# Kernel tuning notes

Measured on AMD Instinct MI355X. Metric: run time of the kernel, lower is better.

The kernel has to match this reference:

```python
import jax, jax.numpy as jnp
import numpy as np

_GELU = lambda x: jax.nn.gelu(x, approximate=False)  # torch nn.GELU default = exact erf


def setup_inputs():
    key = jax.random.key(0)
    ks = jax.random.split(key, 32)
    B, H = 16384, 768
    def p(i, shape):
        return jax.random.normal(ks[i], shape, jnp.float32) * 0.02
    return {
        "image_feat": jax.random.normal(ks[0], (B, H), jnp.float32),
        "text_feat": jax.random.normal(ks[1], (B, H), jnp.float32),
        "enhanced_image_feat": jax.random.normal(ks[2], (B, H), jnp.float32),
        "enhanced_text_feat": jax.random.normal(ks[3], (B, H), jnp.float32),
        "missing_type": jax.random.randint(ks[4], (B,), 0, 4),
        # info_encoder: H->256->64
        "info_w1": p(5, (H, 256)), "info_b1": jnp.zeros((256,), jnp.float32),
        "info_w2": p(6, (256, 64)), "info_b2": jnp.zeros((64,), jnp.float32),
        # modality_importance_predictor: H->H/2->1 (dropout inactive at eval)
        "imp_w1": p(7, (H, H // 2)), "imp_b1": jnp.zeros((H // 2,), jnp.float32),
        "imp_w2": p(8, (H // 2, 1)), "imp_b2": jnp.zeros((1,), jnp.float32),
        # feature_discriminator: H->256->64->1
        "disc_w1": p(9, (H, 256)), "disc_b1": jnp.zeros((256,), jnp.float32),
        "disc_w2": p(10, (256, 64)), "disc_b2": jnp.zeros((64,), jnp.float32),
        "disc_w3": p(11, (64, 1)), "disc_b3": jnp.zeros((1,), jnp.float32),
        # consistency_predictor: 2H->H->H/2->1
        "cons_w1": p(12, (2 * H, H)), "cons_b1": jnp.zeros((H,), jnp.float32),
        "cons_w2": p(13, (H, H // 2)), "cons_b2": jnp.zeros((H // 2,), jnp.float32),
        "cons_w3": p(14, (H // 2, 1)), "cons_b3": jnp.zeros((1,), jnp.float32),
        # task_difficulty_predictor: 2H->H->H/2->1
        "diff_w1": p(15, (2 * H, H)), "diff_b1": jnp.zeros((H,), jnp.float32),
        "diff_w2": p(16, (H, H // 2)), "diff_b2": jnp.zeros((H // 2,), jnp.float32),
        "diff_w3": p(17, (H // 2, 1)), "diff_b3": jnp.zeros((1,), jnp.float32),
    }


def _forward(image_feat, text_feat, enhanced_image_feat, enhanced_text_feat,
             info_w1, info_b1, info_w2, info_b2,
             imp_w1, imp_b1, imp_w2, imp_b2,
             disc_w1, disc_b1, disc_w2, disc_b2, disc_w3, disc_b3,
             cons_w1, cons_b1, cons_w2, cons_b2, cons_w3, cons_b3,
             diff_w1, diff_b1, diff_w2, diff_b2, diff_w3, diff_b3):
    sig = jax.nn.sigmoid

    def geometric(f):  # vectorized version of the per-sample python loop
        n = jnp.linalg.norm(f, axis=-1)
        nq = sig((n - 1.0) * 2.0)
        sp = jnp.mean((jnp.abs(f) > 0.01).astype(jnp.float32), axis=-1)
        sq = sig(jnp.std(f, axis=-1, ddof=1) * 10.0 - 1.0)  # torch.std is unbiased
        return (nq + sp + sq) / 3.0

    def information(f):
        enc = _GELU(f @ info_w1 + info_b1) @ info_w2 + info_b2  # [B,64]
        disc = jnp.round(sig(enc) * 10.0).astype(jnp.int32)     # values in 0..10
        # histogram-based entropy == the torch.unique loop (prob = count/64)
        counts = jnp.sum(disc[:, :, None] == jnp.arange(11, dtype=jnp.int32)[None, None, :], axis=1)
        prob = counts.astype(jnp.float32) / enc.shape[-1]
        ent = -jnp.sum(jnp.where(prob > 0, prob * jnp.log(prob + 1e-8), 0.0), axis=-1)
        eq = sig(ent - 2.0)
        # svd of a 1xD matrix has a single singular value = ||f||_2
        n = jnp.linalg.norm(f, axis=-1)
        cq = (n > 0.01).astype(jnp.float32) / f.shape[-1]
        fn = f / jnp.maximum(n, 1e-12)[:, None]  # F.normalize
        dq = sig(jnp.sum(fn * fn, axis=-1) - 0.5)
        return (eq + cq + dq) / 3.0

    def importance(f):
        return sig(_GELU(f @ imp_w1 + imp_b1) @ imp_w2 + imp_b2)[:, 0]

    def discrim(f):
        h = _GELU(f @ disc_w1 + disc_b1)
        h = _GELU(h @ disc_w2 + disc_b2)
        return sig(h @ disc_w3 + disc_b3)[:, 0]

    def head3(f, w1, b1, w2, b2, w3, b3):
        h = _GELU(f @ w1 + b1)
        h = _GELU(h @ w2 + b2)
        return sig(h @ w3 + b3)[:, 0]

    g_img = geometric(image_feat)
    g_txt = geometric(text_feat)
    g_eimg = geometric(enhanced_image_feat)
    g_etxt = geometric(enhanced_text_feat)
    i_img = information(image_feat)
    i_txt = information(text_feat)
    cons_o = head3(jnp.concatenate([image_feat, text_feat], -1), cons_w1, cons_b1, cons_w2, cons_b2, cons_w3, cons_b3)
    cons_e = head3(jnp.concatenate([enhanced_image_feat, enhanced_text_feat], -1), cons_w1, cons_b1, cons_w2, cons_b2, cons_w3, cons_b3)
    imp_i = importance(image_feat)
    imp_t = importance(text_feat)
    imp_ei = importance(enhanced_image_feat)
    imp_et = importance(enhanced_text_feat)
    auth_io = discrim(image_feat)
    auth_ie = discrim(enhanced_image_feat)
    auth_to = discrim(text_feat)
    auth_te = discrim(enhanced_text_feat)
    diff = head3(jnp.concatenate([enhanced_image_feat, enhanced_text_feat], -1), diff_w1, diff_b1, diff_w2, diff_b2, diff_w3, diff_b3)
    overall = (g_img + g_txt + i_img + i_txt + cons_e + (imp_i + imp_t) / 2.0) / 6.0
    return jnp.stack([g_img, g_txt, g_eimg, g_etxt, i_img, i_txt, cons_o, cons_e,
                      imp_i, imp_t, imp_ei, imp_et, auth_io, auth_ie, auth_to, auth_te,
                      diff, overall])  # [18, B]


def reference(image_feat, text_feat, enhanced_image_feat, enhanced_text_feat, missing_type,
              info_w1, info_b1, info_w2, info_b2,
              imp_w1, imp_b1, imp_w2, imp_b2,
              disc_w1, disc_b1, disc_w2, disc_b2, disc_w3, disc_b3,
              cons_w1, cons_b1, cons_w2, cons_b2, cons_w3, cons_b3,
              diff_w1, diff_b1, diff_w2, diff_b2, diff_w3, diff_b3):
    # missing_type is carried by the original forward but never used in the math
    return _forward(image_feat, text_feat, enhanced_image_feat, enhanced_text_feat,
                    info_w1, info_b1, info_w2, info_b2,
                    imp_w1, imp_b1, imp_w2, imp_b2,
                    disc_w1, disc_b1, disc_w2, disc_b2, disc_w3, disc_b3,
                    cons_w1, cons_b1, cons_w2, cons_b2, cons_w3, cons_b3,
                    diff_w1, diff_b1, diff_w2, diff_b2, diff_w3, diff_b3)
```

## Files before the change

kernel.cpp:

```cpp
#include <hip/hip_runtime.h>

typedef unsigned short bfu;
typedef __attribute__((ext_vector_type(8))) __bf16 bf16x8;
typedef __attribute__((ext_vector_type(4))) float f32x4;

__device__ __forceinline__ float bf2f(bfu u) {
    unsigned int x = ((unsigned int)u) << 16;
    return __builtin_bit_cast(float, x);
}
__device__ __forceinline__ bfu f2bf(float f) {
    unsigned int u = __builtin_bit_cast(unsigned int, f);
    unsigned int r = (u + 0x7fffu + ((u >> 16) & 1u)) >> 16;
    return (bfu)r;
}
__device__ __forceinline__ float sigm(float x) { return 1.0f / (1.0f + __expf(-x)); }
__device__ __forceinline__ float gelu_f(float x) {
    const float y = 0.7978845608f * (x + 0.044715f * x * x * x);
    const float t = 1.f - 2.f / (__expf(2.f * y) + 1.f);
    return 0.5f * x * (1.f + t);
}
__device__ __forceinline__ float gelu_x(float x) {
    return 0.5f * x * (1.0f + erff(x * 0.70710678118654752f));
}

__device__ __forceinline__ void async16(const void* g, void* l) {
    __builtin_amdgcn_global_load_lds((const __attribute__((address_space(1))) void*)g,
                                     (__attribute__((address_space(3))) void*)l, 16, 0, 0);
}

struct TDesc { const float* src; bfu* dst; int K, N, blk0; };
struct TPack { TDesc d[9]; };

__global__ __launch_bounds__(256) void transpose_k(TPack p) {
    const int bid = blockIdx.x;
    int j = 0;
#pragma unroll
    for (int i = 1; i < 9; ++i)
        if (bid >= p.d[i].blk0) j = i;
    const TDesc d = p.d[j];
    const int local = bid - d.blk0;
    const int tkn = d.K >> 6;
    const int tk = local % tkn, tn = local / tkn;
    const int k0 = tk * 64, n0 = tn * 64;
    __shared__ float tile[64][65];
    const int tx = threadIdx.x & 63, ty = threadIdx.x >> 6;
#pragma unroll
    for (int i = 0; i < 16; ++i) {
        const int r = ty * 16 + i;
        tile[r][tx] = d.src[(size_t)(k0 + r) * d.N + n0 + tx];
    }
    __syncthreads();
#pragma unroll
    for (int i = 0; i < 16; ++i) {
        const int n = ty * 16 + i;
        d.dst[(size_t)(n0 + n) * d.K + k0 + tx] = f2bf(tile[tx][n]);
    }
}

__global__ __launch_bounds__(256)
void geomcast_k(const float* F0, const float* F1, bfu* D0, bfu* D1,
                float* g0, float* g1, float* p0, float* p1) {
    const int z = blockIdx.y;
    const float* F = z ? F1 : F0;
    bfu* D = z ? D1 : D0;
    float* gout = z ? g1 : g0;
    float* part = z ? p1 : p0;
    const int wave = threadIdx.x >> 6, lane = threadIdx.x & 63;
    const int row = blockIdx.x * 4 + wave;
    const float* fr = F + (size_t)row * 768;
    bfu* dr = D + (size_t)row * 768;
    float sum = 0.f, ss = 0.f, cnt = 0.f;
#pragma unroll
    for (int i = 0; i < 3; ++i) {
        const float4 v = *(const float4*)(fr + i * 256 + lane * 4);
        sum += v.x + v.y + v.z + v.w;
        ss += v.x * v.x + v.y * v.y + v.z * v.z + v.w * v.w;
        cnt += ((fabsf(v.x) > 0.01f) ? 1.f : 0.f) + ((fabsf(v.y) > 0.01f) ? 1.f : 0.f) +
               ((fabsf(v.z) > 0.01f) ? 1.f : 0.f) + ((fabsf(v.w) > 0.01f) ? 1.f : 0.f);
        ushort4 b;
        b.x = f2bf(v.x); b.y = f2bf(v.y); b.z = f2bf(v.z); b.w = f2bf(v.w);
        *(ushort4*)(dr + i * 256 + lane * 4) = b;
    }
#pragma unroll
    for (int off = 32; off; off >>= 1) {
        sum += __shfl_xor(sum, off);
        ss  += __shfl_xor(ss, off);
        cnt += __shfl_xor(cnt, off);
    }
    if (lane == 0) {
        const float n = sqrtf(ss);
        const float nq = sigm((n - 1.f) * 2.f);
        const float sp = cnt * (1.f / 768.f);
        float var = (ss - sum * sum * (1.f / 768.f)) * (1.f / 767.f);
        var = fmaxf(var, 0.f);
        const float sq = sigm(sqrtf(var) * 10.f - 1.f);
        gout[row] = (nq + sp + sq) * (1.f / 3.f);
        if (part) {
            const float cq = (n > 0.01f) ? (1.f / 768.f) : 0.f;
            const float nc = fmaxf(n, 1e-12f);
            const float dq = sigm(ss / (nc * nc) - 0.5f);
            part[row] = (cq + dq) * (1.f / 3.f);
        }
    }
}

struct Seg {
    const bfu* A; const bfu* A2;
    const bfu* W;
    const float* bias;
    const float* dotw;
    bfu* C;
    float* acc;
    int ldc; int mode;
};
struct SegPack { Seg s[12]; };

__global__ __launch_bounds__(256)
void gemm_k(SegPack p, int K, int Ksplit, int lda) {
    constexpr int BM = 128, BK = 64, MT = 4, NT = 4;
    __shared__ bfu As[BM * BK];
    __shared__ bfu Ws[128 * BK];
    const int NTt = gridDim.x;
    const int g = blockIdx.y * NTt + blockIdx.x;
    const int G8 = NTt * 8;
    const int m = (g / G8) * 8 + (g & 7);
    const int n = (g % G8) >> 3;
    const Seg sg = p.s[n];
    const int t = threadIdx.x;
    const int wave = t >> 6, lane = t & 63;
    const int row_l = lane & 15, kq = lane >> 4;
    const int m0 = m * BM;
    const int wm = wave >> 1, wn = wave & 1;
    const int wrow0 = wm * 64, wcol0 = wn * 64;

    f32x4 acc[MT][NT] = {};

    const int nkt = K / BK;
    for (int kt = 0; kt < nkt; ++kt) {
        const int k0 = kt * BK;
        const bfu* Ab;
        int kc;
        if (k0 < Ksplit) { Ab = sg.A; kc = k0; }
        else             { Ab = sg.A2; kc = k0 - Ksplit; }
#pragma unroll
        for (int i = 0; i < 4; ++i) {
            const int c = i * 256 + t;
            const int r = c >> 3, s = c & 7;
            const int cc = (s ^ (r & 7)) << 3;
            async16(Ab + (size_t)(m0 + r) * lda + kc + cc, As + ((i * 256 + wave * 64) << 3));
        }
#pragma unroll
        for (int i = 0; i < 4; ++i) {
            const int c = i * 256 + t;
            const int r = c >> 3, s = c & 7;
            const int cc = (s ^ (r & 7)) << 3;
            async16(sg.W + (size_t)r * K + k0 + cc, Ws + ((i * 256 + wave * 64) << 3));
        }
        __syncthreads();
#pragma unroll
        for (int ks = 0; ks < 2; ++ks) {
            bf16x8 af[MT], bfr[NT];
#pragma unroll
            for (int mi = 0; mi < MT; ++mi) {
                const int rA = wrow0 + mi * 16 + row_l;
                af[mi] = *(const bf16x8*)(As + rA * BK + (((ks * 4 + kq) ^ (rA & 7)) << 3));
            }
#pragma unroll
            for (int ni = 0; ni < NT; ++ni) {
                const int rB = wcol0 + ni * 16 + row_l;
                bfr[ni] = *(const bf16x8*)(Ws + rB * BK + (((ks * 4 + kq) ^ (rB & 7)) << 3));
            }
#pragma unroll
            for (int mi = 0; mi < MT; ++mi)
#pragma unroll
                for (int ni = 0; ni < NT; ++ni)
                    acc[mi][ni] = __builtin_amdgcn_mfma_f32_16x16x32_bf16(af[mi], bfr[ni], acc[mi][ni], 0, 0, 0);
        }
        __syncthreads();
    }

    if (sg.mode == 0) {
#pragma unroll
        for (int ni = 0; ni < NT; ++ni) {
            const int col = wcol0 + ni * 16 + row_l;
            const float bv = sg.bias[col];
#pragma unroll
            for (int mi = 0; mi < MT; ++mi)
#pragma unroll
                for (int r = 0; r < 4; ++r) {
                    const int row = m0 + wrow0 + mi * 16 + kq * 4 + r;
                    sg.C[(size_t)row * sg.ldc + col] = f2bf(gelu_f(acc[mi][ni][r] + bv));
                }
        }
    } else if (sg.mode == 2) {
#pragma unroll
        for (int ni = 0; ni < NT; ++ni) {
            const int col = wcol0 + ni * 16 + row_l;
            const float bv = sg.bias[col];
#pragma unroll
            for (int mi = 0; mi < MT; ++mi)
#pragma unroll
                for (int r = 0; r < 4; ++r) {
                    const int row = m0 + wrow0 + mi * 16 + kq * 4 + r;
                    sg.C[(size_t)row * sg.ldc + col] = f2bf(gelu_x(acc[mi][ni][r] + bv));
                }
        }
    } else {
#pragma unroll
        for (int mi = 0; mi < MT; ++mi)
#pragma unroll
            for (int r = 0; r < 4; ++r) {
                float s = 0.f;
#pragma unroll
                for (int ni = 0; ni < NT; ++ni) {
                    const int col = wcol0 + ni * 16 + row_l;
                    s += sg.dotw[col] * gelu_f(acc[mi][ni][r] + sg.bias[col]);
                }
                s += __shfl_xor(s, 1); s += __shfl_xor(s, 2);
                s += __shfl_xor(s, 4); s += __shfl_xor(s, 8);
                if (row_l == 0)
                    atomicAdd(sg.acc + m0 + wrow0 + mi * 16 + kq * 4 + r, s);
            }
    }
}

__global__ __launch_bounds__(256)
void gemm64dot_k(const bfu* __restrict__ A, const bfu* __restrict__ W,
                 const float* __restrict__ bias, const float* __restrict__ dotw,
                 float* acc_out, int K, int lda) {
    constexpr int BK = 64, MT = 2, NT = 4;
    __shared__ bfu As[128 * BK];
    __shared__ bfu Ws[64 * BK];
    const int t = threadIdx.x;
    const int wave = t >> 6, lane = t & 63;
    const int row_l = lane & 15, kq = lane >> 4;
    const int m0 = blockIdx.x * 128;
    const int wrow0 = wave * 32;
    f32x4 acc[MT][NT] = {};
    const int nkt = K / BK;
    for (int kt = 0; kt < nkt; ++kt) {
        const int k0 = kt * BK;
#pragma unroll
        for (int i = 0; i < 4; ++i) {
            const int c = i * 256 + t;
            const int r = c >> 3, s = c & 7;
            const int cc = (s ^ (r & 7)) << 3;
            async16(A + (size_t)(m0 + r) * lda + k0 + cc, As + ((i * 256 + wave * 64) << 3));
        }
#pragma unroll
        for (int i = 0; i < 2; ++i) {
            const int c = i * 256 + t;
            const int r = c >> 3, s = c & 7;
            const int cc = (s ^ (r & 7)) << 3;
            async16(W + (size_t)r * K + k0 + cc, Ws + ((i * 256 + wave * 64) << 3));
        }
        __syncthreads();
#pragma unroll
        for (int ks = 0; ks < 2; ++ks) {
            bf16x8 af[MT], bfr[NT];
#pragma unroll
            for (int mi = 0; mi < MT; ++mi) {
                const int rA = wrow0 + mi * 16 + row_l;
                af[mi] = *(const bf16x8*)(As + rA * BK + (((ks * 4 + kq) ^ (rA & 7)) << 3));
            }
#pragma unroll
            for (int ni = 0; ni < NT; ++ni) {
                const int rB = ni * 16 + row_l;
                bfr[ni] = *(const bf16x8*)(Ws + rB * BK + (((ks * 4 + kq) ^ (rB & 7)) << 3));
            }
#pragma unroll
            for (int mi = 0; mi < MT; ++mi)
#pragma unroll
                for (int ni = 0; ni < NT; ++ni)
                    acc[mi][ni] = __builtin_amdgcn_mfma_f32_16x16x32_bf16(af[mi], bfr[ni], acc[mi][ni], 0, 0, 0);
        }
        __syncthreads();
    }
#pragma unroll
    for (int mi = 0; mi < MT; ++mi)
#pragma unroll
        for (int r = 0; r < 4; ++r) {
            float s = 0.f;
#pragma unroll
            for (int ni = 0; ni < NT; ++ni) {
                const int col = ni * 16 + row_l;
                s += dotw[col] * gelu_f(acc[mi][ni][r] + bias[col]);
            }
            s += __shfl_xor(s, 1); s += __shfl_xor(s, 2);
            s += __shfl_xor(s, 4); s += __shfl_xor(s, 8);
            if (row_l == 0)
                acc_out[m0 + wrow0 + mi * 16 + kq * 4 + r] = s;
        }
}

__global__ __launch_bounds__(256)
void gemm64ent_k(const bfu* __restrict__ A, const bfu* __restrict__ W,
                 const float* __restrict__ bias, const float* __restrict__ part,
                 float* out, int B, int K, int lda) {
    constexpr int BK = 64, MT = 2, NT = 4;
    __shared__ __align__(16) float smemf[8320];
    bfu* As = (bfu*)smemf;
    bfu* Ws = (bfu*)smemf + 128 * BK;
    float* ET = smemf;
    const int t = threadIdx.x;
    const int wave = t >> 6, lane = t & 63;
    const int row_l = lane & 15, kq = lane >> 4;
    const int m0 = blockIdx.x * 128;
    const int wrow0 = wave * 32;
    f32x4 acc[MT][NT] = {};
    const int nkt = K / BK;
    for (int kt = 0; kt < nkt; ++kt) {
        const int k0 = kt * BK;
#pragma unroll
        for (int i = 0; i < 4; ++i) {
            const int c = i * 256 + t;
            const int r = c >> 3, s = c & 7;
            const int cc = (s ^ (r & 7)) << 3;
            async16(A + (size_t)(m0 + r) * lda + k0 + cc, As + ((i * 256 + wave * 64) << 3));
        }
#pragma unroll
        for (int i = 0; i < 2; ++i) {
            const int c = i * 256 + t;
            const int r = c >> 3, s = c & 7;
            const int cc = (s ^ (r & 7)) << 3;
            async16(W + (size_t)r * K + k0 + cc, Ws + ((i * 256 + wave * 64) << 3));
        }
        __syncthreads();
#pragma unroll
        for (int ks = 0; ks < 2; ++ks) {
            bf16x8 af[MT], bfr[NT];
#pragma unroll
            for (int mi = 0; mi < MT; ++mi) {
                const int rA = wrow0 + mi * 16 + row_l;
                af[mi] = *(const bf16x8*)(As + rA * BK + (((ks * 4 + kq) ^ (rA & 7)) << 3));
            }
#pragma unroll
            for (int ni = 0; ni < NT; ++ni) {
                const int rB = ni * 16 + row_l;
                bfr[ni] = *(const bf16x8*)(Ws + rB * BK + (((ks * 4 + kq) ^ (rB & 7)) << 3));
            }
#pragma unroll
            for (int mi = 0; mi < MT; ++mi)
#pragma unroll
                for (int ni = 0; ni < NT; ++ni)
                    acc[mi][ni] = __builtin_amdgcn_mfma_f32_16x16x32_bf16(af[mi], bfr[ni], acc[mi][ni], 0, 0, 0);
        }
        __syncthreads();
    }
#pragma unroll
    for (int mi = 0; mi < MT; ++mi)
#pragma unroll
        for (int ni = 0; ni < NT; ++ni) {
            const int col = ni * 16 + row_l;
            const float bv = bias[col];
#pragma unroll
            for (int r = 0; r < 4; ++r)
                ET[(wrow0 + mi * 16 + kq * 4 + r) * 65 + col] = acc[mi][ni][r] + bv;
        }
    __syncthreads();
    if (t < 128) {
        int cnt[11];
#pragma unroll
        for (int b = 0; b < 11; ++b) cnt[b] = 0;
        for (int j = 0; j < 64; ++j) {
            const int d = (int)rintf(sigm(ET[t * 65 + j]) * 10.f);
#pragma unroll
            for (int b = 0; b < 11; ++b) cnt[b] += (d == b);
        }
        float ent = 0.f;
#pragma unroll
        for (int b = 0; b < 11; ++b) {
            if (cnt[b] > 0) {
                const float pp = (float)cnt[b] * (1.f / 64.f);
                ent -= pp * __logf(pp + 1e-8f);
            }
        }
        const int row = m0 + t;
        const int orow = (row < B) ? 4 : 5;
        const int rl = (row < B) ? row : row - B;
        out[(size_t)orow * B + rl] = part[row] + sigm(ent - 2.f) * (1.f / 3.f);
    }
}

__global__ __launch_bounds__(256) void zero_k(float* p, int n) {
    const int i = blockIdx.x * 256 + threadIdx.x;
    if (i < n) p[i] = 0.f;
}

__global__ __launch_bounds__(256)
void finalize_k(float* out, const float* a_imp1, const float* a_imp2,
                const float* a_co, const float* a_ce, const float* a_df,
                const float* a_d1, const float* a_d2,
                const float* imp_b2, const float* disc_b3,
                const float* cons_b3, const float* diff_b3, int B) {
    const int i = blockIdx.x * 256 + threadIdx.x;
    if (i >= B) return;
    const float ib = imp_b2[0], db = disc_b3[0], cb = cons_b3[0], fb = diff_b3[0];
    const float o6 = sigm(a_co[i] + cb);
    const float o7 = sigm(a_ce[i] + cb);
    const float o8 = sigm(a_imp1[i] + ib);
    const float o9 = sigm(a_imp1[B + i] + ib);
    out[6 * B + i] = o6;
    out[7 * B + i] = o7;
    out[8 * B + i] = o8;
    out[9 * B + i] = o9;
    out[10 * B + i] = sigm(a_imp2[i] + ib);
    out[11 * B + i] = sigm(a_imp2[B + i] + ib);
    out[12 * B + i] = sigm(a_d1[i] + db);
    out[14 * B + i] = sigm(a_d1[B + i] + db);
    out[13 * B + i] = sigm(a_d2[i] + db);
    out[15 * B + i] = sigm(a_d2[B + i] + db);
    out[16 * B + i] = sigm(a_df[i] + fb);
    const float v = out[0 * B + i] + out[1 * B + i] + out[4 * B + i] + out[5 * B + i] +
                    o7 + 0.5f * (o8 + o9);
    out[17 * B + i] = v * (1.f / 6.f);
}

extern "C" void kernel_launch(void* const* d_in, const int* in_sizes, int n_in,
                              void* d_out, int out_size, void* d_ws, size_t ws_size,
                              hipStream_t stream) {
    const int B = in_sizes[4];
    const int B2 = 2 * B;
    float* out = (float*)d_out;
    const float* img  = (const float*)d_in[0];
    const float* txt  = (const float*)d_in[1];
    const float* eimg = (const float*)d_in[2];
    const float* etxt = (const float*)d_in[3];
    const float* info_w1 = (const float*)d_in[5];  const float* info_b1 = (const float*)d_in[6];
    const float* info_w2 = (const float*)d_in[7];  const float* info_b2 = (const float*)d_in[8];
    const float* imp_w1  = (const float*)d_in[9];  const float* imp_b1  = (const float*)d_in[10];
    const float* imp_w2  = (const float*)d_in[11]; const float* imp_b2  = (const float*)d_in[12];
    const float* disc_w1 = (const float*)d_in[13]; const float* disc_b1 = (const float*)d_in[14];
    const float* disc_w2 = (const float*)d_in[15]; const float* disc_b2 = (const float*)d_in[16];
    const float* disc_w3 = (const float*)d_in[17]; const float* disc_b3 = (const float*)d_in[18];
    const float* cons_w1 = (const float*)d_in[19]; const float* cons_b1 = (const float*)d_in[20];
    const float* cons_w2 = (const float*)d_in[21]; const float* cons_b2 = (const float*)d_in[22];
    const float* cons_w3 = (const float*)d_in[23]; const float* cons_b3 = (const float*)d_in[24];
    const float* diff_w1 = (const float*)d_in[25]; const float* diff_b1 = (const float*)d_in[26];
    const float* diff_w2 = (const float*)d_in[27]; const float* diff_b2 = (const float*)d_in[28];
    const float* diff_w3 = (const float*)d_in[29]; const float* diff_b3 = (const float*)d_in[30];

    char* wsp = (char*)d_ws;
    size_t off = 0;
    auto alloc = [&](size_t bytes) -> void* {
        void* p = wsp + off;
        off += (bytes + 255) & ~(size_t)255;
        return p;
    };
    bfu* info1t = (bfu*)alloc((size_t)256 * 768 * 2);
    bfu* info2t = (bfu*)alloc((size_t)64 * 256 * 2);
    bfu* imp1t  = (bfu*)alloc((size_t)384 * 768 * 2);
    bfu* disc1t = (bfu*)alloc((size_t)256 * 768 * 2);
    bfu* disc2t = (bfu*)alloc((size_t)64 * 256 * 2);
    bfu* cons1t = (bfu*)alloc((size_t)768 * 1536 * 2);
    bfu* cons2t = (bfu*)alloc((size_t)384 * 768 * 2);
    bfu* diff1t = (bfu*)alloc((size_t)768 * 1536 * 2);
    bfu* diff2t = (bfu*)alloc((size_t)384 * 768 * 2);
    float* part = (float*)alloc((size_t)B2 * 4);
    float* accz = (float*)alloc((size_t)(7 * B + 4 * B) * 4);
    float* a_imp1 = accz;
    float* a_imp2 = accz + B2;
    float* a_co = accz + 2 * B2;
    float* a_ce = a_co + B;
    float* a_df = a_ce + B;
    float* a_d1 = a_df + B;
    float* a_d2 = a_d1 + B2;
    bfu* fA01 = (bfu*)alloc((size_t)B2 * 768 * 2);
    bfu* X    = (bfu*)alloc((size_t)B2 * 768 * 2);
    bfu* Hi   = X;
    bfu* Hd   = X + (size_t)B2 * 256;
    bfu* Hc_c = X;
    bfu* Hc_d = X + (size_t)B * 768;
    (void)ws_size; (void)n_in; (void)out_size;

    zero_k<<<dim3((7 * B + 255) / 256), 256, 0, stream>>>(accz, 7 * B);

    TPack tp;
    int blk = 0, ti = 0;
    auto setd = [&](const float* s, bfu* d, int K, int N) {
        tp.d[ti++] = {s, d, K, N, blk};
        blk += (K / 64) * (N / 64);
    };
    setd(info_w1, info1t, 768, 256);
    setd(info_w2, info2t, 256, 64);
    setd(imp_w1, imp1t, 768, 384);
    setd(disc_w1, disc1t, 768, 256);
    setd(disc_w2, disc2t, 256, 64);
    setd(cons_w1, cons1t, 1536, 768);
    setd(cons_w2, cons2t, 768, 384);
    setd(diff_w1, diff1t, 1536, 768);
    setd(diff_w2, diff2t, 768, 384);
    transpose_k<<<dim3(blk), 256, 0, stream>>>(tp);

    auto store_seg = [&](const bfu* A, const bfu* A2, const bfu* W, const float* b,
                         bfu* C, int ldc, int mode) -> Seg {
        return Seg{A, A2, W, b, nullptr, C, nullptr, ldc, mode};
    };
    auto dot_seg = [&](const bfu* A, const bfu* A2, const bfu* W, const float* b,
                       const float* dw, float* acc) -> Seg {
        return Seg{A, A2, W, b, dw, nullptr, acc, 0, 1};
    };
    const bfu* fB = fA01 + (size_t)B * 768;

    geomcast_k<<<dim3(B / 4, 2), 256, 0, stream>>>(img, txt, fA01, (bfu*)fB,
                                                   out + 0 * B, out + 1 * B, part, part + B);
    {
        SegPack p;
        p.s[0] = store_seg(fA01, fA01, info1t, info_b1, Hi, 256, 2);
        p.s[1] = store_seg(fA01, fA01, info1t + (size_t)128 * 768, info_b1 + 128, Hi + 128, 256, 2);
        for (int i = 0; i < 3; ++i)
            p.s[2 + i] = dot_seg(fA01, fA01, imp1t + (size_t)128 * i * 768,
                                 imp_b1 + 128 * i, imp_w2 + 128 * i, a_imp1);
        p.s[5] = store_seg(fA01, fA01, disc1t, disc_b1, Hd, 256, 0);
        p.s[6] = store_seg(fA01, fA01, disc1t + (size_t)128 * 768, disc_b1 + 128, Hd + 128, 256, 0);
        for (int i = 7; i < 12; ++i) p.s[i] = p.s[0];
        gemm_k<<<dim3(7, B2 / 128), 256, 0, stream>>>(p, 768, 768, 768);
    }
    gemm64ent_k<<<dim3(B2 / 128), 256, 0, stream>>>(Hi, info2t, info_b2, part, out, B, 256, 256);
    gemm64dot_k<<<dim3(B2 / 128), 256, 0, stream>>>(Hd, disc2t, disc_b2, disc_w3, a_d1, 256, 256);
    {
        SegPack p;
        for (int i = 0; i < 6; ++i)
            p.s[i] = store_seg(fA01, fB, cons1t + (size_t)128 * i * 1536,
                               cons_b1 + 128 * i, Hc_c + 128 * i, 768, 0);
        for (int i = 6; i < 12; ++i) p.s[i] = p.s[0];
        gemm_k<<<dim3(6, B / 128), 256, 0, stream>>>(p, 1536, 768, 768);
    }
    {
        SegPack p;
        for (int i = 0; i < 3; ++i)
            p.s[i] = dot_seg(Hc_c, Hc_c, cons2t + (size_t)128 * i * 768,
                             cons_b2 + 128 * i, cons_w3 + 128 * i, a_co);
        for (int i = 3; i < 12; ++i) p.s[i] = p.s[0];
        gemm_k<<<dim3(3, B / 128), 256, 0, stream>>>(p, 768, 768, 768);
    }

    geomcast_k<<<dim3(B / 4, 2), 256, 0, stream>>>(eimg, etxt, fA01, (bfu*)fB,
                                                   out + 2 * B, out + 3 * B, nullptr, nullptr);
    {
        SegPack p;
        for (int i = 0; i < 3; ++i)
            p.s[i] = dot_seg(fA01, fA01, imp1t + (size_t)128 * i * 768,
                             imp_b1 + 128 * i, imp_w2 + 128 * i, a_imp2);
        p.s[3] = store_seg(fA01, fA01, disc1t, disc_b1, Hd, 256, 0);
        p.s[4] = store_seg(fA01, fA01, disc1t + (size_t)128 * 768, disc_b1 + 128, Hd + 128, 256, 0);
        for (int i = 5; i < 12; ++i) p.s[i] = p.s[0];
        gemm_k<<<dim3(5, B2 / 128), 256, 0, stream>>>(p, 768, 768, 768);
    }
    gemm64dot_k<<<dim3(B2 / 128), 256, 0, stream>>>(Hd, disc2t, disc_b2, disc_w3, a_d2, 256, 256);
    {
        SegPack p;
        for (int i = 0; i < 6; ++i) {
            p.s[i]     = store_seg(fA01, fB, cons1t + (size_t)128 * i * 1536,
                                   cons_b1 + 128 * i, Hc_c + 128 * i, 768, 0);
            p.s[6 + i] = store_seg(fA01, fB, diff1t + (size_t)128 * i * 1536,
                                   diff_b1 + 128 * i, Hc_d + 128 * i, 768, 0);
        }
        gemm_k<<<dim3(12, B / 128), 256, 0, stream>>>(p, 1536, 768, 768);
    }
    {
        SegPack p;
        for (int i = 0; i < 3; ++i) {
            p.s[i]     = dot_seg(Hc_c, Hc_c, cons2t + (size_t)128 * i * 768,
                                 cons_b2 + 128 * i, cons_w3 + 128 * i, a_ce);
            p.s[3 + i] = dot_seg(Hc_d, Hc_d, diff2t + (size_t)128 * i * 768,
                                 diff_b2 + 128 * i, diff_w3 + 128 * i, a_df);
        }
        for (int i = 6; i < 12; ++i) p.s[i] = p.s[0];
        gemm_k<<<dim3(6, B / 128), 256, 0, stream>>>(p, 768, 768, 768);
    }

    finalize_k<<<dim3((B + 255) / 256), 256, 0, stream>>>(out, a_imp1, a_imp2, a_co, a_ce,
                                                          a_df, a_d1, a_d2,
                                                          imp_b2, disc_b3, cons_b3, diff_b3, B);
}
```

Before: 730.5 us.

## Merge GEMM launches via per-segment shapes and fold disc layer-2 into grouped GEMM

Each segment now carries its own K, Ksplit, lda and M-tile count, so independent GEMMs with different shapes share one grouped launch. The small disc layer-2 GEMM goes into the grouped kernel by padding its weights to 128 columns. The cons layer-2 dot is moved into the later enhanced-feature launch, and the intermediate buffers are laid out so they do not alias. The goal is fewer launches and fewer low-occupancy phases. The cost is blocks that exit early for M-tiles past a segment's limit, plus wasted compute on the padded disc columns. Address computation in the K loop is also simplified to pointer increments.

```diff
diff --git a/kernel.cpp b/kernel.cpp
--- a/kernel.cpp
+++ b/kernel.cpp
@@ -54,6 +54,18 @@
     for (int i = 0; i < 16; ++i) {
         const int n = ty * 16 + i;
         d.dst[(size_t)(n0 + n) * d.K + k0 + tx] = f2bf(tile[tx][n]);
+    }
+}
+
+__global__ __launch_bounds__(256)
+void prep_k(float* accz, int nacc, bfu* disc2pad, const float* w3,
+            const float* b2, float* w3pad, float* b2pad) {
+    const int i = blockIdx.x * 256 + threadIdx.x;
+    if (i < nacc) accz[i] = 0.f;
+    if (i < 64 * 256) disc2pad[64 * 256 + i] = 0;
+    if (i < 128) {
+        w3pad[i] = (i < 64) ? w3[i] : 0.f;
+        b2pad[i] = (i < 64) ? b2[i] : 0.f;
     }
 }
 
@@ -111,14 +123,14 @@
     const float* dotw;
     bfu* C;
     float* acc;
-    int ldc; int mode;
+    int ldc, mode, K, Ksplit, lda, Mtiles;
 };
-struct SegPack { Seg s[12]; };
+struct SegPack { Seg s[13]; };
 
 __global__ __launch_bounds__(256)
-void gemm_k(SegPack p, int K, int Ksplit, int lda) {
-    constexpr int BM = 128, BK = 64, MT = 4, NT = 4;
-    __shared__ bfu As[BM * BK];
+void gemm_k(SegPack p) {
+    constexpr int BK = 64, MT = 4, NT = 4;
+    __shared__ bfu As[128 * BK];
     __shared__ bfu Ws[128 * BK];
     const int NTt = gridDim.x;
     const int g = blockIdx.y * NTt + blockIdx.x;
@@ -126,36 +138,42 @@
     const int m = (g / G8) * 8 + (g & 7);
     const int n = (g % G8) >> 3;
     const Seg sg = p.s[n];
+    if (m >= sg.Mtiles) return;
     const int t = threadIdx.x;
     const int wave = t >> 6, lane = t & 63;
     const int row_l = lane & 15, kq = lane >> 4;
-    const int m0 = m * BM;
+    const int m0 = m * 128;
     const int wm = wave >> 1, wn = wave & 1;
     const int wrow0 = wm * 64, wcol0 = wn * 64;
 
+    const int r0 = t >> 3;
+    const int cc = ((t & 7) ^ (r0 & 7)) << 3;
+    const size_t strA = (size_t)32 * sg.lda;
+    const size_t strW = (size_t)32 * sg.K;
+    const bfu* pA[4];
+    const bfu* pW[4];
+#pragma unroll
+    for (int i = 0; i < 4; ++i) {
+        pA[i] = sg.A + (size_t)(m0 + r0) * sg.lda + cc + i * strA;
+        pW[i] = sg.W + (size_t)r0 * sg.K + cc + i * strW;
+    }
+    const int nkt = sg.K >> 6;
+    const int ktsw = (sg.Ksplit < sg.K) ? (sg.Ksplit >> 6) : 0x7fffffff;
+
     f32x4 acc[MT][NT] = {};
 
-    const int nkt = K / BK;
     for (int kt = 0; kt < nkt; ++kt) {
-        const int k0 = kt * BK;
-        const bfu* Ab;
-        int kc;
-        if (k0 < Ksplit) { Ab = sg.A; kc = k0; }
-        else             { Ab = sg.A2; kc = k0 - Ksplit; }
-#pragma unroll
-        for (int i = 0; i < 4; ++i) {
-            const int c = i * 256 + t;
-            const int r = c >> 3, s = c & 7;
-            const int cc = (s ^ (r & 7)) << 3;
-            async16(Ab + (size_t)(m0 + r) * lda + kc + cc, As + ((i * 256 + wave * 64) << 3));
-        }
-#pragma unroll
-        for (int i = 0; i < 4; ++i) {
-            const int c = i * 256 + t;
-            const int r = c >> 3, s = c & 7;
-            const int cc = (s ^ (r & 7)) << 3;
-            async16(sg.W + (size_t)r * K + k0 + cc, Ws + ((i * 256 + wave * 64) << 3));
-        }
+        if (kt == ktsw) {
+#pragma unroll
+            for (int i = 0; i < 4; ++i)
+                pA[i] = sg.A2 + (size_t)(m0 + r0) * sg.lda + cc + i * strA;
+        }
+#pragma unroll
+        for (int i = 0; i < 4; ++i)
+            async16(pA[i], As + ((i * 256 + wave * 64) << 3));
+#pragma unroll
+        for (int i = 0; i < 4; ++i)
+            async16(pW[i], Ws + ((i * 256 + wave * 64) << 3));
         __syncthreads();
 #pragma unroll
         for (int ks = 0; ks < 2; ++ks) {
@@ -177,6 +195,8 @@
                     acc[mi][ni] = __builtin_amdgcn_mfma_f32_16x16x32_bf16(af[mi], bfr[ni], acc[mi][ni], 0, 0, 0);
         }
         __syncthreads();
+#pragma unroll
+        for (int i = 0; i < 4; ++i) { pA[i] += BK; pW[i] += BK; }
     }
 
     if (sg.mode == 0) {
@@ -222,75 +242,6 @@
                     atomicAdd(sg.acc + m0 + wrow0 + mi * 16 + kq * 4 + r, s);
             }
     }
-}
-
-__global__ __launch_bounds__(256)
-void gemm64dot_k(const bfu* __restrict__ A, const bfu* __restrict__ W,
-                 const float* __restrict__ bias, const float* __restrict__ dotw,
-                 float* acc_out, int K, int lda) {
-    constexpr int BK = 64, MT = 2, NT = 4;
-    __shared__ bfu As[128 * BK];
-    __shared__ bfu Ws[64 * BK];
-    const int t = threadIdx.x;
-    const int wave = t >> 6, lane = t & 63;
-    const int row_l = lane & 15, kq = lane >> 4;
-    const int m0 = blockIdx.x * 128;
-    const int wrow0 = wave * 32;
-    f32x4 acc[MT][NT] = {};
-    const int nkt = K / BK;
-    for (int kt = 0; kt < nkt; ++kt) {
-        const int k0 = kt * BK;
-#pragma unroll
-        for (int i = 0; i < 4; ++i) {
-            const int c = i * 256 + t;
-            const int r = c >> 3, s = c & 7;
-            const int cc = (s ^ (r & 7)) << 3;
-            async16(A + (size_t)(m0 + r) * lda + k0 + cc, As + ((i * 256 + wave * 64) << 3));
-        }
-#pragma unroll
-        for (int i = 0; i < 2; ++i) {
-            const int c = i * 256 + t;
-            const int r = c >> 3, s = c & 7;
-            const int cc = (s ^ (r & 7)) << 3;
-            async16(W + (size_t)r * K + k0 + cc, Ws + ((i * 256 + wave * 64) << 3));
-        }
-        __syncthreads();
-#pragma unroll
-        for (int ks = 0; ks < 2; ++ks) {
-            bf16x8 af[MT], bfr[NT];
-#pragma unroll
-            for (int mi = 0; mi < MT; ++mi) {
-                const int rA = wrow0 + mi * 16 + row_l;
-                af[mi] = *(const bf16x8*)(As + rA * BK + (((ks * 4 + kq) ^ (rA & 7)) << 3));
-            }
-#pragma unroll
-            for (int ni = 0; ni < NT; ++ni) {
-                const int rB = ni * 16 + row_l;
-                bfr[ni] = *(const bf16x8*)(Ws + rB * BK + (((ks * 4 + kq) ^ (rB & 7)) << 3));
-            }
-#pragma unroll
-            for (int mi = 0; mi < MT; ++mi)
-#pragma unroll
-                for (int ni = 0; ni < NT; ++ni)
-                    acc[mi][ni] = __builtin_amdgcn_mfma_f32_16x16x32_bf16(af[mi], bfr[ni], acc[mi][ni], 0, 0, 0);
-        }
-        __syncthreads();
-    }
-#pragma unroll
-    for (int mi = 0; mi < MT; ++mi)
-#pragma unroll
-        for (int r = 0; r < 4; ++r) {
-            float s = 0.f;
-#pragma unroll
-            for (int ni = 0; ni < NT; ++ni) {
-                const int col = ni * 16 + row_l;
-                s += dotw[col] * gelu_f(acc[mi][ni][r] + bias[col]);
-            }
-            s += __shfl_xor(s, 1); s += __shfl_xor(s, 2);
-            s += __shfl_xor(s, 4); s += __shfl_xor(s, 8);
-            if (row_l == 0)
-                acc_out[m0 + wrow0 + mi * 16 + kq * 4 + r] = s;
-        }
 }
 
 __global__ __launch_bounds__(256)
@@ -380,11 +331,6 @@
         const int rl = (row < B) ? row : row - B;
         out[(size_t)orow * B + rl] = part[row] + sigm(ent - 2.f) * (1.f / 3.f);
     }
-}
-
-__global__ __launch_bounds__(256) void zero_k(float* p, int n) {
-    const int i = blockIdx.x * 256 + threadIdx.x;
-    if (i < n) p[i] = 0.f;
 }
 
 __global__ __launch_bounds__(256)
@@ -451,13 +397,15 @@
     bfu* info2t = (bfu*)alloc((size_t)64 * 256 * 2);
     bfu* imp1t  = (bfu*)alloc((size_t)384 * 768 * 2);
     bfu* disc1t = (bfu*)alloc((size_t)256 * 768 * 2);
-    bfu* disc2t = (bfu*)alloc((size_t)64 * 256 * 2);
+    bfu* disc2p = (bfu*)alloc((size_t)128 * 256 * 2);
     bfu* cons1t = (bfu*)alloc((size_t)768 * 1536 * 2);
     bfu* cons2t = (bfu*)alloc((size_t)384 * 768 * 2);
     bfu* diff1t = (bfu*)alloc((size_t)768 * 1536 * 2);
     bfu* diff2t = (bfu*)alloc((size_t)384 * 768 * 2);
+    float* w3pad = (float*)alloc(128 * 4);
+    float* b2pad = (float*)alloc(128 * 4);
     float* part = (float*)alloc((size_t)B2 * 4);
-    float* accz = (float*)alloc((size_t)(7 * B + 4 * B) * 4);
+    float* accz = (float*)alloc((size_t)11 * B * 4);
     float* a_imp1 = accz;
     float* a_imp2 = accz + B2;
     float* a_co = accz + 2 * B2;
@@ -466,15 +414,15 @@
     float* a_d1 = a_df + B;
     float* a_d2 = a_d1 + B2;
     bfu* fA01 = (bfu*)alloc((size_t)B2 * 768 * 2);
-    bfu* X    = (bfu*)alloc((size_t)B2 * 768 * 2);
-    bfu* Hi   = X;
-    bfu* Hd   = X + (size_t)B2 * 256;
-    bfu* Hc_c = X;
-    bfu* Hc_d = X + (size_t)B * 768;
+    bfu* X    = (bfu*)alloc((size_t)B * 2048 * 2);
+    bfu* Hd   = X;
+    bfu* Hi   = X + (size_t)B * 512;
+    bfu* Hc_c = X + (size_t)B * 512;
+    bfu* Hc_d = X + (size_t)B * 1280;
     (void)ws_size; (void)n_in; (void)out_size;
 
-    zero_k<<<dim3((7 * B + 255) / 256), 256, 0, stream>>>(accz, 7 * B);
-
+    prep_k<<<dim3((11 * B + 255) / 256), 256, 0, stream>>>(accz, 11 * B, disc2p,
+                                                           disc_w3, disc_b2, w3pad, b2pad);
     TPack tp;
     int blk = 0, ti = 0;
     auto setd = [&](const float* s, bfu* d, int K, int N) {
@@ -485,54 +433,45 @@
     setd(info_w2, info2t, 256, 64);
     setd(imp_w1, imp1t, 768, 384);
     setd(disc_w1, disc1t, 768, 256);
-    setd(disc_w2, disc2t, 256, 64);
+    setd(disc_w2, disc2p, 256, 64);
     setd(cons_w1, cons1t, 1536, 768);
     setd(cons_w2, cons2t, 768, 384);
     setd(diff_w1, diff1t, 1536, 768);
     setd(diff_w2, diff2t, 768, 384);
     transpose_k<<<dim3(blk), 256, 0, stream>>>(tp);
 
-    auto store_seg = [&](const bfu* A, const bfu* A2, const bfu* W, const float* b,
-                         bfu* C, int ldc, int mode) -> Seg {
-        return Seg{A, A2, W, b, nullptr, C, nullptr, ldc, mode};
+    auto st_seg = [&](const bfu* A, const bfu* A2, const bfu* W, const float* b,
+                      bfu* C, int ldc, int mode, int K, int Ksplit, int lda, int Mt) -> Seg {
+        return Seg{A, A2, W, b, nullptr, C, nullptr, ldc, mode, K, Ksplit, lda, Mt};
     };
-    auto dot_seg = [&](const bfu* A, const bfu* A2, const bfu* W, const float* b,
-                       const float* dw, float* acc) -> Seg {
-        return Seg{A, A2, W, b, dw, nullptr, acc, 0, 1};
+    auto dt_seg = [&](const bfu* A, const bfu* W, const float* b, const float* dw,
+                      float* acc, int K, int lda, int Mt) -> Seg {
+        return Seg{A, nullptr, W, b, dw, nullptr, acc, 0, 1, K, K, lda, Mt};
     };
     const bfu* fB = fA01 + (size_t)B * 768;
+    const int MT2 = B2 / 128, MT1 = B / 128;
 
     geomcast_k<<<dim3(B / 4, 2), 256, 0, stream>>>(img, txt, fA01, (bfu*)fB,
                                                    out + 0 * B, out + 1 * B, part, part + B);
     {
         SegPack p;
-        p.s[0] = store_seg(fA01, fA01, info1t, info_b1, Hi, 256, 2);
-        p.s[1] = store_seg(fA01, fA01, info1t + (size_t)128 * 768, info_b1 + 128, Hi + 128, 256, 2);
+        p.s[0] = st_seg(fA01, nullptr, info1t, info_b1, Hi, 256, 2, 768, 768, 768, MT2);
+        p.s[1] = st_seg(fA01, nullptr, info1t + (size_t)128 * 768, info_b1 + 128, Hi + 128, 256, 2, 768, 768, 768, MT2);
         for (int i = 0; i < 3; ++i)
-            p.s[2 + i] = dot_seg(fA01, fA01, imp1t + (size_t)128 * i * 768,
-                                 imp_b1 + 128 * i, imp_w2 + 128 * i, a_imp1);
-        p.s[5] = store_seg(fA01, fA01, disc1t, disc_b1, Hd, 256, 0);
-        p.s[6] = store_seg(fA01, fA01, disc1t + (size_t)128 * 768, disc_b1 + 128, Hd + 128, 256, 0);
-        for (int i = 7; i < 12; ++i) p.s[i] = p.s[0];
-        gemm_k<<<dim3(7, B2 / 128), 256, 0, stream>>>(p, 768, 768, 768);
-    }
-    gemm64ent_k<<<dim3(B2 / 128), 256, 0, stream>>>(Hi, info2t, info_b2, part, out, B, 256, 256);
-    gemm64dot_k<<<dim3(B2 / 128), 256, 0, stream>>>(Hd, disc2t, disc_b2, disc_w3, a_d1, 256, 256);
+            p.s[2 + i] = dt_seg(fA01, imp1t + (size_t)128 * i * 768, imp_b1 + 128 * i,
+                                imp_w2 + 128 * i, a_imp1, 768, 768, MT2);
+        p.s[5] = st_seg(fA01, nullptr, disc1t, disc_b1, Hd, 256, 0, 768, 768, 768, MT2);
+        p.s[6] = st_seg(fA01, nullptr, disc1t + (size_t)128 * 768, disc_b1 + 128, Hd + 128, 256, 0, 768, 768, 768, MT2);
+        gemm_k<<<dim3(7, MT2), 256, 0, stream>>>(p);
+    }
+    gemm64ent_k<<<dim3(MT2), 256, 0, stream>>>(Hi, info2t, info_b2, part, out, B, 256, 256);
     {
         SegPack p;
+        p.s[0] = dt_seg(Hd, disc2p, b2pad, w3pad, a_d1, 256, 256, MT2);
         for (int i = 0; i < 6; ++i)
-            p.s[i] = store_seg(fA01, fB, cons1t + (size_t)128 * i * 1536,
-                               cons_b1 + 128 * i, Hc_c + 128 * i, 768, 0);
-        for (int i = 6; i < 12; ++i) p.s[i] = p.s[0];
-        gemm_k<<<dim3(6, B / 128), 256, 0, stream>>>(p, 1536, 768, 768);
-    }
-    {
-        SegPack p;
-        for (int i = 0; i < 3; ++i)
-            p.s[i] = dot_seg(Hc_c, Hc_c, cons2t + (size_t)128 * i * 768,
-                             cons_b2 + 128 * i, cons_w3 + 128 * i, a_co);
-        for (int i = 3; i < 12; ++i) p.s[i] = p.s[0];
-        gemm_k<<<dim3(3, B / 128), 256, 0, stream>>>(p, 768, 768, 768);
+            p.s[1 + i] = st_seg(fA01, fB, cons1t + (size_t)128 * i * 1536,
+                                cons_b1 + 128 * i, Hc_c + 128 * i, 768, 0, 1536, 768, 768, MT1);
+        gemm_k<<<dim3(7, MT2), 256, 0, stream>>>(p);
     }
 
     geomcast_k<<<dim3(B / 4, 2), 256, 0, stream>>>(eimg, etxt, fA01, (bfu*)fB,
@@ -540,34 +479,35 @@
     {
         SegPack p;
         for (int i = 0; i < 3; ++i)
-            p.s[i] = dot_seg(fA01, fA01, imp1t + (size_t)128 * i * 768,
-                             imp_b1 + 128 * i, imp_w2 + 128 * i, a_imp2);
-        p.s[3] = store_seg(fA01, fA01, disc1t, disc_b1, Hd, 256, 0);
-        p.s[4] = store_seg(fA01, fA01, disc1t + (size_t)128 * 768, disc_b1 + 128, Hd + 128, 256, 0);
-        for (int i = 5; i < 12; ++i) p.s[i] = p.s[0];
-        gemm_k<<<dim3(5, B2 / 128), 256, 0, stream>>>(p, 768, 768, 768);
-    }
-    gemm64dot_k<<<dim3(B2 / 128), 256, 0, stream>>>(Hd, disc2t, disc_b2, disc_w3, a_d2, 256, 256);
+            p.s[i] = dt_seg(fA01, imp1t + (size_t)128 * i * 768, imp_b1 + 128 * i,
+                            imp_w2 + 128 * i, a_imp2, 768, 768, MT2);
+        p.s[3] = st_seg(fA01, nullptr, disc1t, disc_b1, Hd, 256, 0, 768, 768, 768, MT2);
+        p.s[4] = st_seg(fA01, nullptr, disc1t + (size_t)128 * 768, disc_b1 + 128, Hd + 128, 256, 0, 768, 768, 768, MT2);
+        for (int i = 0; i < 3; ++i)
+            p.s[5 + i] = dt_seg(Hc_c, cons2t + (size_t)128 * i * 768, cons_b2 + 128 * i,
+                                cons_w3 + 128 * i, a_co, 768, 768, MT1);
+        gemm_k<<<dim3(8, MT2), 256, 0, stream>>>(p);
+    }
     {
         SegPack p;
+        p.s[0] = dt_seg(Hd, disc2p, b2pad, w3pad, a_d2, 256, 256, MT2);
         for (int i = 0; i < 6; ++i) {
-            p.s[i]     = store_seg(fA01, fB, cons1t + (size_t)128 * i * 1536,
-                                   cons_b1 + 128 * i, Hc_c + 128 * i, 768, 0);
-            p.s[6 + i] = store_seg(fA01, fB, diff1t + (size_t)128 * i * 1536,
-                                   diff_b1 + 128 * i, Hc_d + 128 * i, 768, 0);
-        }
-        gemm_k<<<dim3(12, B / 128), 256, 0, stream>>>(p, 1536, 768, 768);
+            p.s[1 + i] = st_seg(fA01, fB, cons1t + (size_t)128 * i * 1536,
+                                cons_b1 + 128 * i, Hc_c + 128 * i, 768, 0, 1536, 768, 768, MT1);
+            p.s[7 + i] = st_seg(fA01, fB, diff1t + (size_t)128 * i * 1536,
+                                diff_b1 + 128 * i, Hc_d + 128 * i, 768, 0, 1536, 768, 768, MT1);
+        }
+        gemm_k<<<dim3(13, MT2), 256, 0, stream>>>(p);
     }
     {
         SegPack p;
         for (int i = 0; i < 3; ++i) {
-            p.s[i]     = dot_seg(Hc_c, Hc_c, cons2t + (size_t)128 * i * 768,
-                                 cons_b2 + 128 * i, cons_w3 + 128 * i, a_ce);
-            p.s[3 + i] = dot_seg(Hc_d, Hc_d, diff2t + (size_t)128 * i * 768,
-                                 diff_b2 + 128 * i, diff_w3 + 128 * i, a_df);
-        }
-        for (int i = 6; i < 12; ++i) p.s[i] = p.s[0];
-        gemm_k<<<dim3(6, B / 128), 256, 0, stream>>>(p, 768, 768, 768);
+            p.s[i]     = dt_seg(Hc_c, cons2t + (size_t)128 * i * 768, cons_b2 + 128 * i,
+                                cons_w3 + 128 * i, a_ce, 768, 768, MT1);
+            p.s[3 + i] = dt_seg(Hc_d, diff2t + (size_t)128 * i * 768, diff_b2 + 128 * i,
+                                diff_w3 + 128 * i, a_df, 768, 768, MT1);
+        }
+        gemm_k<<<dim3(6, MT1), 256, 0, stream>>>(p);
     }
 
     finalize_k<<<dim3((B + 255) / 256), 256, 0, stream>>>(out, a_imp1, a_imp2, a_co, a_ce,
```

After: 724.3 us. Within noise of the previous version (-0.8%).
